# Kernel optimization log

Hardware: AMD Instinct MI355X
Metric: run time of the kernel (lower is better)

Reference implementation:

```python
import jax, jax.numpy as jnp
import numpy as np

BETA = 1.0  # cfg.TRAINING.beta
B, S, D = 128, 256, 1024


def setup_inputs() -> dict:
    key = jax.random.key(0)
    k1, k2, k3 = jax.random.split(key, 3)
    bridges = jax.random.normal(k1, (B, S, D), dtype=jnp.float32)
    # monotone increasing timestamps per row (true_divide-safe: bt>bp>bh)
    b_inx = jnp.arange(B * S, dtype=jnp.int32).reshape(B, S)
    # negative indices: one per positive position j in [1, S-2];
    # (idx + 1 + r) % dim guarantees neg_i != i and neg_j != j
    neg_i = (jnp.arange(B, dtype=jnp.int32)[:, None] + 1
             + jax.random.randint(k2, (B, S - 2), 0, B - 1, dtype=jnp.int32)) % B
    neg_j = (jnp.arange(1, S - 1, dtype=jnp.int32)[None, :] + 1
             + jax.random.randint(k3, (B, S - 2), 0, S - 1, dtype=jnp.int32)) % S
    return {"bridges": bridges, "b_inx": b_inx, "neg_i": neg_i, "neg_j": neg_j}


def reference(bridges, b_inx, neg_i, neg_j):
    dt = bridges.dtype
    t = b_inx.astype(dt)
    th = t[:, :1]            # [B,1] head timestamp
    tt = t[:, -1:]           # [B,1] tail timestamp
    tp = t[:, 1:-1]          # [B,S-2] positive timestamps
    alpha = (tp - th) / (tt - th)          # [B,S-2]
    sigma = alpha * (tt - tp)              # [B,S-2]

    head = bridges[:, 0]                   # [B,D]
    tail = bridges[:, -1]                  # [B,D]
    pos = bridges[:, 1:-1]                 # [B,S-2,D]
    neg = bridges[neg_i, neg_j]            # [B,S-2,D]

    a = alpha[..., None]
    mix = (1.0 - a) * head[:, None, :] + a * tail[:, None, :]  # [B,S-2,D]
    xp = pos - mix
    xn = neg - mix
    inv = 1.0 / (2.0 * sigma * sigma)
    pos_dis = -jnp.sum(xp * xp, axis=-1) * inv   # -||x||^2 / (2 sigma^2)
    neg_dis = -jnp.sum(xn * xn, axis=-1) * inv

    cur = pos_dis - neg_dis + jnp.asarray(BETA, dt)
    loss = jnp.sum(jnp.where(cur > 0, cur, jnp.zeros((), dt)))
    return loss / bridges.shape[0]
```

## Files before the change

### kernel.cpp

```cpp
#include <hip/hip_runtime.h>

constexpr int   Bc   = 128;
constexpr int   Sc   = 256;
constexpr int   Dc   = 1024;
constexpr float BETA = 1.0f;
constexpr int   NP   = Bc * (Sc - 2);
constexpr int   NR   = Bc * Sc;
constexpr int   CAP  = 32;

constexpr size_t OFF_CNT  = 0;
constexpr size_t OFF_OVFC = 131072;
constexpr size_t OFF_LIST = 131200;
constexpr size_t OFF_OVFL = OFF_LIST + (size_t)NR * CAP * 4;
constexpr size_t OFF_POS  = OFF_OVFL + (size_t)NP * 4;
constexpr size_t OFF_NEG  = OFF_POS  + (size_t)NP * 4;

__global__ __launch_bounds__(256) void k_build(
    const int* __restrict__ neg_i, const int* __restrict__ neg_j,
    int* __restrict__ cnt, int* __restrict__ list,
    int* __restrict__ ovf_cnt, int* __restrict__ ovf_list)
{
    const int p = blockIdx.x * 256 + threadIdx.x;
    const int b = p / (Sc - 2);
    const int j = p - b * (Sc - 2);
    const int r = neg_i[p] * Sc + neg_j[p];
    const int slot = atomicAdd(&cnt[r], 1);
    if (slot < CAP) {
        list[r * CAP + slot] = (b << 8) | j;
    } else {
        ovf_list[atomicAdd(ovf_cnt, 1)] = p;
    }
}

__global__ __launch_bounds__(256) void k_main(
    const float* __restrict__ bridges, const int* __restrict__ b_inx,
    const int* __restrict__ cnt, const int* __restrict__ list,
    float* __restrict__ pos_dis, float* __restrict__ neg_dis)
{
    const int r    = (blockIdx.x * 256 + threadIdx.x) >> 6;
    const int lane = threadIdx.x & 63;
    const int b    = r >> 8;
    const int s    = r & 255;

    const float4* __restrict__ row4 = (const float4*)bridges;

    float4 x[4];
    {
        const float4* rp = row4 + (size_t)r * (Dc / 4);
#pragma unroll
        for (int k = 0; k < 4; ++k) x[k] = rp[k * 64 + lane];
    }

    const int nneg = min(cnt[r], CAP);

    if (s >= 1 && s <= Sc - 2) {
        const float th = (float)b_inx[b * Sc];
        const float tt = (float)b_inx[b * Sc + (Sc - 1)];
        const float tp = (float)b_inx[b * Sc + s];
        const float alpha = (tp - th) / (tt - th);
        const float sigma = alpha * (tt - tp);
        const float inv   = 1.0f / (2.0f * sigma * sigma);
        const float4* hp = row4 + (size_t)(b * Sc) * (Dc / 4);
        const float4* tq = row4 + (size_t)(b * Sc + Sc - 1) * (Dc / 4);
        float d = 0.0f;
#pragma unroll
        for (int k = 0; k < 4; ++k) {
            const float4 h = hp[k * 64 + lane];
            const float4 t = tq[k * 64 + lane];
            const float m0 = fmaf(alpha, t.x - h.x, h.x);
            const float m1 = fmaf(alpha, t.y - h.y, h.y);
            const float m2 = fmaf(alpha, t.z - h.z, h.z);
            const float m3 = fmaf(alpha, t.w - h.w, h.w);
            const float e0 = x[k].x - m0, e1 = x[k].y - m1;
            const float e2 = x[k].z - m2, e3 = x[k].w - m3;
            d += e0 * e0 + e1 * e1 + e2 * e2 + e3 * e3;
        }
#pragma unroll
        for (int m = 32; m >= 1; m >>= 1) d += __shfl_xor(d, m);
        if (lane == 0) pos_dis[b * (Sc - 2) + (s - 1)] = -d * inv;
    }

    for (int q = 0; q < nneg; ++q) {
        const int e  = list[r * CAP + q];
        const int bb = e >> 8;
        const int jj = e & 255;
        const int ss = jj + 1;
        const float th = (float)b_inx[bb * Sc];
        const float tt = (float)b_inx[bb * Sc + (Sc - 1)];
        const float tp = (float)b_inx[bb * Sc + ss];
        const float alpha = (tp - th) / (tt - th);
        const float sigma = alpha * (tt - tp);
        const float inv   = 1.0f / (2.0f * sigma * sigma);
        const float4* hp = row4 + (size_t)(bb * Sc) * (Dc / 4);
        const float4* tq = row4 + (size_t)(bb * Sc + Sc - 1) * (Dc / 4);
        float d = 0.0f;
#pragma unroll
        for (int k = 0; k < 4; ++k) {
            const float4 h = hp[k * 64 + lane];
            const float4 t = tq[k * 64 + lane];
            const float m0 = fmaf(alpha, t.x - h.x, h.x);
            const float m1 = fmaf(alpha, t.y - h.y, h.y);
            const float m2 = fmaf(alpha, t.z - h.z, h.z);
            const float m3 = fmaf(alpha, t.w - h.w, h.w);
            const float e0 = x[k].x - m0, e1 = x[k].y - m1;
            const float e2 = x[k].z - m2, e3 = x[k].w - m3;
            d += e0 * e0 + e1 * e1 + e2 * e2 + e3 * e3;
        }
#pragma unroll
        for (int m = 32; m >= 1; m >>= 1) d += __shfl_xor(d, m);
        if (lane == 0) neg_dis[bb * (Sc - 2) + jj] = -d * inv;
    }
}

__global__ __launch_bounds__(1024) void k_reduce(
    const float* __restrict__ bridges, const int* __restrict__ b_inx,
    const int* __restrict__ neg_i, const int* __restrict__ neg_j,
    const int* __restrict__ ovf_cnt, const int* __restrict__ ovf_list,
    const float* __restrict__ pos_dis, float* __restrict__ neg_dis,
    float* __restrict__ out)
{
    const int t    = threadIdx.x;
    const int wave = t >> 6;
    const int lane = t & 63;
    const float4* __restrict__ row4 = (const float4*)bridges;

    const int novf = *ovf_cnt;
    for (int e = wave; e < novf; e += 16) {
        const int p  = ovf_list[e];
        const int bb = p / (Sc - 2);
        const int jj = p - bb * (Sc - 2);
        const int ss = jj + 1;
        const int r  = neg_i[p] * Sc + neg_j[p];
        const float th = (float)b_inx[bb * Sc];
        const float tt = (float)b_inx[bb * Sc + (Sc - 1)];
        const float tp = (float)b_inx[bb * Sc + ss];
        const float alpha = (tp - th) / (tt - th);
        const float sigma = alpha * (tt - tp);
        const float inv   = 1.0f / (2.0f * sigma * sigma);
        const float4* xp = row4 + (size_t)r * (Dc / 4);
        const float4* hp = row4 + (size_t)(bb * Sc) * (Dc / 4);
        const float4* tq = row4 + (size_t)(bb * Sc + Sc - 1) * (Dc / 4);
        float d = 0.0f;
#pragma unroll
        for (int k = 0; k < 4; ++k) {
            const float4 x = xp[k * 64 + lane];
            const float4 h = hp[k * 64 + lane];
            const float4 tv = tq[k * 64 + lane];
            const float m0 = fmaf(alpha, tv.x - h.x, h.x);
            const float m1 = fmaf(alpha, tv.y - h.y, h.y);
            const float m2 = fmaf(alpha, tv.z - h.z, h.z);
            const float m3 = fmaf(alpha, tv.w - h.w, h.w);
            const float e0 = x.x - m0, e1 = x.y - m1;
            const float e2 = x.z - m2, e3 = x.w - m3;
            d += e0 * e0 + e1 * e1 + e2 * e2 + e3 * e3;
        }
#pragma unroll
        for (int m = 32; m >= 1; m >>= 1) d += __shfl_xor(d, m);
        if (lane == 0) neg_dis[bb * (Sc - 2) + jj] = -d * inv;
    }
    __syncthreads();

    __shared__ float red[1024];
    float a = 0.0f;
    for (int p = t; p < NP; p += 1024) {
        const float cur = pos_dis[p] - neg_dis[p] + BETA;
        if (cur > 0.0f) a += cur;
    }
    red[t] = a;
    __syncthreads();
    for (int d = 512; d > 0; d >>= 1) {
        if (t < d) red[t] += red[t + d];
        __syncthreads();
    }
    if (t == 0) out[0] = red[0] * (1.0f / (float)Bc);
}

extern "C" void kernel_launch(void* const* d_in, const int* in_sizes, int n_in,
                              void* d_out, int out_size, void* d_ws, size_t ws_size,
                              hipStream_t stream) {
    const float* bridges = (const float*)d_in[0];
    const int*   b_inx   = (const int*)d_in[1];
    const int*   neg_i   = (const int*)d_in[2];
    const int*   neg_j   = (const int*)d_in[3];
    float*       out     = (float*)d_out;

    char* ws = (char*)d_ws;
    int*   cnt      = (int*)(ws + OFF_CNT);
    int*   ovf_cnt  = (int*)(ws + OFF_OVFC);
    int*   list     = (int*)(ws + OFF_LIST);
    int*   ovf_list = (int*)(ws + OFF_OVFL);
    float* pos_dis  = (float*)(ws + OFF_POS);
    float* neg_dis  = (float*)(ws + OFF_NEG);

    hipMemsetAsync(ws, 0, OFF_OVFC + 4, stream);
    k_build <<<NP / 256, 256, 0, stream>>>(neg_i, neg_j, cnt, list, ovf_cnt, ovf_list);
    k_main  <<<NR / 4, 256, 0, stream>>>(bridges, b_inx, cnt, list, pos_dis, neg_dis);
    k_reduce<<<1, 1024, 0, stream>>>(bridges, b_inx, neg_i, neg_j,
                                     ovf_cnt, ovf_list, pos_dis, neg_dis, out);
}
```

Measured before the change: 217.9 us.

## Precompute per-pair params in build, prefetch records, parallelize hinge reduction

The build kernel now computes alpha and inv once per pair and stores them, for positives in a param array and inline in 16-byte negative records, so k_main no longer reads b_inx or does divides per pair, and the next record is prefetched. The per-row list capacity drops to 8. Overflowed negatives are flagged with INFINITY in neg_dis and recomputed serially per thread inside a new multi-block hinge kernel, which replaces the single-block reduction and uses atomicAdd into the output. This removes the serial single-block tail, but overflow recompute is a slow scalar 1024-element loop per thread, and float atomic accumulation is nondeterministic.

```diff
diff --git a/kernel.cpp b/kernel.cpp
--- a/kernel.cpp
+++ b/kernel.cpp
@@ -1,40 +1,52 @@
 #include <hip/hip_runtime.h>
+#include <math.h>
 
 constexpr int   Bc   = 128;
 constexpr int   Sc   = 256;
 constexpr int   Dc   = 1024;
 constexpr float BETA = 1.0f;
-constexpr int   NP   = Bc * (Sc - 2);
+constexpr int   SP   = Sc - 2;
+constexpr int   NP   = Bc * SP;
 constexpr int   NR   = Bc * Sc;
-constexpr int   CAP  = 32;
+constexpr int   CAP  = 8;
 
 constexpr size_t OFF_CNT  = 0;
-constexpr size_t OFF_OVFC = 131072;
-constexpr size_t OFF_LIST = 131200;
-constexpr size_t OFF_OVFL = OFF_LIST + (size_t)NR * CAP * 4;
-constexpr size_t OFF_POS  = OFF_OVFL + (size_t)NP * 4;
-constexpr size_t OFF_NEG  = OFF_POS  + (size_t)NP * 4;
+constexpr size_t OFF_REC  = 131072;
+constexpr size_t OFF_PPAR = OFF_REC + (size_t)NR * CAP * 16;
+constexpr size_t OFF_PD   = OFF_PPAR + (size_t)NP * 8;
+constexpr size_t OFF_ND   = OFF_PD + (size_t)NP * 4;
 
 __global__ __launch_bounds__(256) void k_build(
-    const int* __restrict__ neg_i, const int* __restrict__ neg_j,
-    int* __restrict__ cnt, int* __restrict__ list,
-    int* __restrict__ ovf_cnt, int* __restrict__ ovf_list)
+    const int* __restrict__ b_inx, const int* __restrict__ neg_i,
+    const int* __restrict__ neg_j, int* __restrict__ cnt,
+    float4* __restrict__ rec, float2* __restrict__ ppar,
+    float* __restrict__ neg_dis, float* __restrict__ out)
 {
     const int p = blockIdx.x * 256 + threadIdx.x;
-    const int b = p / (Sc - 2);
-    const int j = p - b * (Sc - 2);
+    if (p == 0) out[0] = 0.0f;
+    const int b = p / SP;
+    const int j = p - b * SP;
+    const int s = j + 1;
+    const float th = (float)b_inx[b * Sc];
+    const float tt = (float)b_inx[b * Sc + (Sc - 1)];
+    const float tp = (float)b_inx[b * Sc + s];
+    const float alpha = (tp - th) / (tt - th);
+    const float sigma = alpha * (tt - tp);
+    const float inv   = 1.0f / (2.0f * sigma * sigma);
+    ppar[p] = make_float2(alpha, inv);
     const int r = neg_i[p] * Sc + neg_j[p];
     const int slot = atomicAdd(&cnt[r], 1);
     if (slot < CAP) {
-        list[r * CAP + slot] = (b << 8) | j;
+        rec[r * CAP + slot] = make_float4(__int_as_float((b << 8) | j), alpha, inv, 0.0f);
     } else {
-        ovf_list[atomicAdd(ovf_cnt, 1)] = p;
+        neg_dis[p] = INFINITY;
     }
 }
 
 __global__ __launch_bounds__(256) void k_main(
-    const float* __restrict__ bridges, const int* __restrict__ b_inx,
-    const int* __restrict__ cnt, const int* __restrict__ list,
+    const float* __restrict__ bridges,
+    const int* __restrict__ cnt, const float4* __restrict__ rec,
+    const float2* __restrict__ ppar,
     float* __restrict__ pos_dis, float* __restrict__ neg_dis)
 {
     const int r    = (blockIdx.x * 256 + threadIdx.x) >> 6;
@@ -52,16 +64,14 @@
     }
 
     const int nneg = min(cnt[r], CAP);
+    float4 rc = rec[r * CAP];
+
+    const float4* hp = row4 + (size_t)(b * Sc) * (Dc / 4);
+    const float4* tq = row4 + (size_t)(b * Sc + Sc - 1) * (Dc / 4);
 
     if (s >= 1 && s <= Sc - 2) {
-        const float th = (float)b_inx[b * Sc];
-        const float tt = (float)b_inx[b * Sc + (Sc - 1)];
-        const float tp = (float)b_inx[b * Sc + s];
-        const float alpha = (tp - th) / (tt - th);
-        const float sigma = alpha * (tt - tp);
-        const float inv   = 1.0f / (2.0f * sigma * sigma);
-        const float4* hp = row4 + (size_t)(b * Sc) * (Dc / 4);
-        const float4* tq = row4 + (size_t)(b * Sc + Sc - 1) * (Dc / 4);
+        const float2 pp    = ppar[b * SP + (s - 1)];
+        const float  alpha = pp.x, inv = pp.y;
         float d = 0.0f;
 #pragma unroll
         for (int k = 0; k < 4; ++k) {
@@ -77,27 +87,22 @@
         }
 #pragma unroll
         for (int m = 32; m >= 1; m >>= 1) d += __shfl_xor(d, m);
-        if (lane == 0) pos_dis[b * (Sc - 2) + (s - 1)] = -d * inv;
+        if (lane == 0) pos_dis[b * SP + (s - 1)] = -d * inv;
     }
 
     for (int q = 0; q < nneg; ++q) {
-        const int e  = list[r * CAP + q];
-        const int bb = e >> 8;
-        const int jj = e & 255;
-        const int ss = jj + 1;
-        const float th = (float)b_inx[bb * Sc];
-        const float tt = (float)b_inx[bb * Sc + (Sc - 1)];
-        const float tp = (float)b_inx[bb * Sc + ss];
-        const float alpha = (tp - th) / (tt - th);
-        const float sigma = alpha * (tt - tp);
-        const float inv   = 1.0f / (2.0f * sigma * sigma);
-        const float4* hp = row4 + (size_t)(bb * Sc) * (Dc / 4);
-        const float4* tq = row4 + (size_t)(bb * Sc + Sc - 1) * (Dc / 4);
+        const int   e     = __float_as_int(rc.x);
+        const float alpha = rc.y, inv = rc.z;
+        const int   bb = e >> 8;
+        const int   jj = e & 255;
+        const float4* hb = row4 + (size_t)(bb * Sc) * (Dc / 4);
+        const float4* tb = row4 + (size_t)(bb * Sc + Sc - 1) * (Dc / 4);
+        if (q + 1 < nneg) rc = rec[r * CAP + q + 1];
         float d = 0.0f;
 #pragma unroll
         for (int k = 0; k < 4; ++k) {
-            const float4 h = hp[k * 64 + lane];
-            const float4 t = tq[k * 64 + lane];
+            const float4 h = hb[k * 64 + lane];
+            const float4 t = tb[k * 64 + lane];
             const float m0 = fmaf(alpha, t.x - h.x, h.x);
             const float m1 = fmaf(alpha, t.y - h.y, h.y);
             const float m2 = fmaf(alpha, t.z - h.z, h.z);
@@ -108,71 +113,52 @@
         }
 #pragma unroll
         for (int m = 32; m >= 1; m >>= 1) d += __shfl_xor(d, m);
-        if (lane == 0) neg_dis[bb * (Sc - 2) + jj] = -d * inv;
+        if (lane == 0) neg_dis[bb * SP + jj] = -d * inv;
     }
 }
 
-__global__ __launch_bounds__(1024) void k_reduce(
+__global__ __launch_bounds__(256) void k_hinge(
     const float* __restrict__ bridges, const int* __restrict__ b_inx,
     const int* __restrict__ neg_i, const int* __restrict__ neg_j,
-    const int* __restrict__ ovf_cnt, const int* __restrict__ ovf_list,
-    const float* __restrict__ pos_dis, float* __restrict__ neg_dis,
+    const float* __restrict__ pos_dis, const float* __restrict__ neg_dis,
     float* __restrict__ out)
 {
-    const int t    = threadIdx.x;
-    const int wave = t >> 6;
-    const int lane = t & 63;
-    const float4* __restrict__ row4 = (const float4*)bridges;
-
-    const int novf = *ovf_cnt;
-    for (int e = wave; e < novf; e += 16) {
-        const int p  = ovf_list[e];
-        const int bb = p / (Sc - 2);
-        const int jj = p - bb * (Sc - 2);
-        const int ss = jj + 1;
-        const int r  = neg_i[p] * Sc + neg_j[p];
-        const float th = (float)b_inx[bb * Sc];
-        const float tt = (float)b_inx[bb * Sc + (Sc - 1)];
-        const float tp = (float)b_inx[bb * Sc + ss];
-        const float alpha = (tp - th) / (tt - th);
-        const float sigma = alpha * (tt - tp);
-        const float inv   = 1.0f / (2.0f * sigma * sigma);
-        const float4* xp = row4 + (size_t)r * (Dc / 4);
-        const float4* hp = row4 + (size_t)(bb * Sc) * (Dc / 4);
-        const float4* tq = row4 + (size_t)(bb * Sc + Sc - 1) * (Dc / 4);
-        float d = 0.0f;
-#pragma unroll
-        for (int k = 0; k < 4; ++k) {
-            const float4 x = xp[k * 64 + lane];
-            const float4 h = hp[k * 64 + lane];
-            const float4 tv = tq[k * 64 + lane];
-            const float m0 = fmaf(alpha, tv.x - h.x, h.x);
-            const float m1 = fmaf(alpha, tv.y - h.y, h.y);
-            const float m2 = fmaf(alpha, tv.z - h.z, h.z);
-            const float m3 = fmaf(alpha, tv.w - h.w, h.w);
-            const float e0 = x.x - m0, e1 = x.y - m1;
-            const float e2 = x.z - m2, e3 = x.w - m3;
-            d += e0 * e0 + e1 * e1 + e2 * e2 + e3 * e3;
+    float a = 0.0f;
+    for (int p = blockIdx.x * 256 + threadIdx.x; p < NP; p += gridDim.x * 256) {
+        float nd = neg_dis[p];
+        if (__builtin_isinf(nd)) {
+            const int bb = p / SP, jj = p - bb * SP, ss = jj + 1;
+            const int r  = neg_i[p] * Sc + neg_j[p];
+            const float th = (float)b_inx[bb * Sc];
+            const float tt = (float)b_inx[bb * Sc + (Sc - 1)];
+            const float tp = (float)b_inx[bb * Sc + ss];
+            const float alpha = (tp - th) / (tt - th);
+            const float sigma = alpha * (tt - tp);
+            const float inv   = 1.0f / (2.0f * sigma * sigma);
+            const float* xr = bridges + (size_t)r * Dc;
+            const float* hr = bridges + (size_t)(bb * Sc) * Dc;
+            const float* tr = bridges + (size_t)(bb * Sc + Sc - 1) * Dc;
+            float d = 0.0f;
+            for (int k = 0; k < Dc; ++k) {
+                const float h = hr[k];
+                const float m = fmaf(alpha, tr[k] - h, h);
+                const float e = xr[k] - m;
+                d += e * e;
+            }
+            nd = -d * inv;
         }
-#pragma unroll
-        for (int m = 32; m >= 1; m >>= 1) d += __shfl_xor(d, m);
-        if (lane == 0) neg_dis[bb * (Sc - 2) + jj] = -d * inv;
-    }
-    __syncthreads();
-
-    __shared__ float red[1024];
-    float a = 0.0f;
-    for (int p = t; p < NP; p += 1024) {
-        const float cur = pos_dis[p] - neg_dis[p] + BETA;
+        const float cur = pos_dis[p] - nd + BETA;
         if (cur > 0.0f) a += cur;
     }
-    red[t] = a;
+    __shared__ float red[4];
+#pragma unroll
+    for (int m = 32; m >= 1; m >>= 1) a += __shfl_xor(a, m);
+    if ((threadIdx.x & 63) == 0) red[threadIdx.x >> 6] = a;
     __syncthreads();
-    for (int d = 512; d > 0; d >>= 1) {
-        if (t < d) red[t] += red[t + d];
-        __syncthreads();
+    if (threadIdx.x == 0) {
+        const float ssum = red[0] + red[1] + red[2] + red[3];
+        atomicAdd(out, ssum * (1.0f / (float)Bc));
     }
-    if (t == 0) out[0] = red[0] * (1.0f / (float)Bc);
 }
 
 extern "C" void kernel_launch(void* const* d_in, const int* in_sizes, int n_in,
@@ -185,16 +171,14 @@
     float*       out     = (float*)d_out;
 
     char* ws = (char*)d_ws;
-    int*   cnt      = (int*)(ws + OFF_CNT);
-    int*   ovf_cnt  = (int*)(ws + OFF_OVFC);
-    int*   list     = (int*)(ws + OFF_LIST);
-    int*   ovf_list = (int*)(ws + OFF_OVFL);
-    float* pos_dis  = (float*)(ws + OFF_POS);
-    float* neg_dis  = (float*)(ws + OFF_NEG);
+    int*    cnt     = (int*)(ws + OFF_CNT);
+    float4* rec     = (float4*)(ws + OFF_REC);
+    float2* ppar    = (float2*)(ws + OFF_PPAR);
+    float*  pos_dis = (float*)(ws + OFF_PD);
+    float*  neg_dis = (float*)(ws + OFF_ND);
 
-    hipMemsetAsync(ws, 0, OFF_OVFC + 4, stream);
-    k_build <<<NP / 256, 256, 0, stream>>>(neg_i, neg_j, cnt, list, ovf_cnt, ovf_list);
-    k_main  <<<NR / 4, 256, 0, stream>>>(bridges, b_inx, cnt, list, pos_dis, neg_dis);
-    k_reduce<<<1, 1024, 0, stream>>>(bridges, b_inx, neg_i, neg_j,
-                                     ovf_cnt, ovf_list, pos_dis, neg_dis, out);
+    hipMemsetAsync(cnt, 0, NR * sizeof(int), stream);
+    k_build<<<NP / 256, 256, 0, stream>>>(b_inx, neg_i, neg_j, cnt, rec, ppar, neg_dis, out);
+    k_main <<<NR / 4, 256, 0, stream>>>(bridges, cnt, rec, ppar, pos_dis, neg_dis);
+    k_hinge<<<128, 256, 0, stream>>>(bridges, b_inx, neg_i, neg_j, pos_dis, neg_dis, out);
 }
```

Measured after the change: 208.0 us. 1.05x faster.
